# Kernel optimization log

Measured on AMD Instinct MI355X. Metric: run time of the kernel, lower is better.

Reference implementation:

```python
import jax, jax.numpy as jnp
import numpy as np

N = 50000   # n_nodes
E = 800000  # n_edges (avg degree 16)
D = 128     # d_model == hidden_dim
N_LAYERS = 3


def _xavier(key, fan_in, fan_out):
    limit = float(np.sqrt(6.0 / (fan_in + fan_out)))
    return jax.random.uniform(key, (fan_in, fan_out), jnp.float32, -limit, limit)


def setup_inputs() -> dict:
    key = jax.random.key(0)
    ks = jax.random.split(key, 2 + 2 * N_LAYERS)
    x = jax.random.normal(ks[0], (N, D), jnp.float32)
    edge_index = jax.random.randint(ks[1], (2, E), 0, N, jnp.int32)
    inp = {"x": x, "edge_index": edge_index}
    for i in range(N_LAYERS):
        inp[f"W{i}"] = _xavier(ks[2 + 2 * i], D, D)
        inp[f"b{i}"] = jax.random.uniform(ks[3 + 2 * i], (D,), jnp.float32, -0.1, 0.1)
    return inp


def _gcn_forward(x, src, dst, norm, Ws, bs):
    n = x.shape[0]
    h = x
    for i, (W, b) in enumerate(zip(Ws, bs)):
        m = (h @ W)[src] * norm[:, None]                       # [E+N, D] gather + scale
        h = jax.ops.segment_sum(m, dst, num_segments=n) + b    # scatter-add aggregate
        if i < len(Ws) - 1:
            h = jax.nn.relu(h)
    return h + x                                               # residual


def reference(x, edge_index, W0, b0, W1, b1, W2, b2):
    n = x.shape[0]
    loop = jnp.arange(n, dtype=edge_index.dtype)
    src = jnp.concatenate([edge_index[0], loop])  # add self-loops (GCNConv default)
    dst = jnp.concatenate([edge_index[1], loop])
    deg = jax.ops.segment_sum(jnp.ones_like(dst, x.dtype), dst, num_segments=n)
    dinv = jax.lax.rsqrt(deg)                     # deg >= 1 due to self-loops
    norm = dinv[src] * dinv[dst]                  # symmetric GCN normalization
    return _gcn_forward(x, src, dst, norm, (W0, W1, W2), (b0, b1, b2))
```

## Files before the change

kernel.cpp:

```cpp
#include <hip/hip_runtime.h>
#include <hip/hip_bf16.h>

#define D 128
#define BCAP 64


__device__ __forceinline__ unsigned short f2bf_rtne(float f) {
    unsigned int u = __float_as_uint(f);
    u += 0x7fffu + ((u >> 16) & 1u);
    return (unsigned short)(u >> 16);
}

__device__ __forceinline__ float bf_lo(unsigned int u) { return __uint_as_float(u << 16); }
__device__ __forceinline__ float bf_hi(unsigned int u) { return __uint_as_float(u & 0xffff0000u); }


__global__ void fill_bucket_kernel(const int* __restrict__ src, const int* __restrict__ dst,
                                   int* __restrict__ cnt, int* __restrict__ bucket, int E) {
    int e = blockIdx.x * blockDim.x + threadIdx.x;
    if (e >= E) return;
    int s = src[e];
    int d = dst[e];
    int pos = atomicAdd(&cnt[d], 1);
    if (pos < BCAP) bucket[((size_t)d << 6) + pos] = s;
}

__global__ void dinv_kernel(const int* __restrict__ cnt, float* __restrict__ dinv, int n) {
    int i = blockIdx.x * blockDim.x + threadIdx.x;
    if (i < n) dinv[i] = rsqrtf((float)cnt[i] + 1.0f);
}


#define TM 64

__global__ __launch_bounds__(256) void gemm128_kernel(const float* __restrict__ h,
                                                      const float* __restrict__ W,
                                                      unsigned short* __restrict__ out, int n) {
    __shared__ float sh[TM * D];
    const int tid = threadIdx.x;
    const int nbase = blockIdx.x * TM;

#pragma unroll
    for (int i = 0; i < 8; ++i) {
        int fi = tid + i * 256;
        int node = nbase + (fi >> 5);
        float4 v = make_float4(0.f, 0.f, 0.f, 0.f);
        if (node < n) v = *(const float4*)&h[(size_t)node * D + ((fi & 31) << 2)];
        *(float4*)&sh[fi << 2] = v;
    }
    __syncthreads();

    const int c4 = (tid & 31) << 2;
    const int ng = tid >> 5;
    const float* shb = &sh[(ng * 8) * D];

    float4 acc[8];
#pragma unroll
    for (int j = 0; j < 8; ++j) acc[j] = make_float4(0.f, 0.f, 0.f, 0.f);

    for (int k = 0; k < D; k += 4) {
        float4 w0 = *(const float4*)&W[(size_t)(k + 0) * D + c4];
        float4 w1 = *(const float4*)&W[(size_t)(k + 1) * D + c4];
        float4 w2 = *(const float4*)&W[(size_t)(k + 2) * D + c4];
        float4 w3 = *(const float4*)&W[(size_t)(k + 3) * D + c4];
#pragma unroll
        for (int j = 0; j < 8; ++j) {
            float4 hv = *(const float4*)&shb[j * D + k];
            acc[j].x = fmaf(hv.x, w0.x, acc[j].x); acc[j].y = fmaf(hv.x, w0.y, acc[j].y);
            acc[j].z = fmaf(hv.x, w0.z, acc[j].z); acc[j].w = fmaf(hv.x, w0.w, acc[j].w);
            acc[j].x = fmaf(hv.y, w1.x, acc[j].x); acc[j].y = fmaf(hv.y, w1.y, acc[j].y);
            acc[j].z = fmaf(hv.y, w1.z, acc[j].z); acc[j].w = fmaf(hv.y, w1.w, acc[j].w);
            acc[j].x = fmaf(hv.z, w2.x, acc[j].x); acc[j].y = fmaf(hv.z, w2.y, acc[j].y);
            acc[j].z = fmaf(hv.z, w2.z, acc[j].z); acc[j].w = fmaf(hv.z, w2.w, acc[j].w);
            acc[j].x = fmaf(hv.w, w3.x, acc[j].x); acc[j].y = fmaf(hv.w, w3.y, acc[j].y);
            acc[j].z = fmaf(hv.w, w3.z, acc[j].z); acc[j].w = fmaf(hv.w, w3.w, acc[j].w);
        }
    }

#pragma unroll
    for (int j = 0; j < 8; ++j) {
        int node = nbase + ng * 8 + j;
        if (node < n) {
            ushort4 p;
            p.x = f2bf_rtne(acc[j].x);
            p.y = f2bf_rtne(acc[j].y);
            p.z = f2bf_rtne(acc[j].z);
            p.w = f2bf_rtne(acc[j].w);
            *(ushort4*)&out[(size_t)node * D + c4] = p;
        }
    }
}


__global__ __launch_bounds__(256) void gather_kernel(const int* __restrict__ cnt,
                                                     const int* __restrict__ bucket,
                                                     const unsigned short* __restrict__ hW,
                                                     const float* __restrict__ dinv,
                                                     const float* __restrict__ b,
                                                     const float* __restrict__ x,
                                                     float* __restrict__ out,
                                                     int n, int final_layer) {
    int node = blockIdx.x * 8 + (threadIdx.x >> 5);
    if (node >= n) return;
    const int f = (threadIdx.x & 31) << 2;
    const int* row = bucket + ((size_t)node << 6);
    int len = cnt[node];
    if (len > BCAP) len = BCAP;
    const int len8 = len & ~7;

    float4 acc0 = make_float4(0.f, 0.f, 0.f, 0.f);
    float4 acc1 = make_float4(0.f, 0.f, 0.f, 0.f);
    int k = 0;
    for (; k < len8; k += 8) {
        int4 sa = *(const int4*)&row[k];
        int4 sb = *(const int4*)&row[k + 4];
        float n0 = dinv[sa.x], n1 = dinv[sa.y], n2 = dinv[sa.z], n3 = dinv[sa.w];
        float n4 = dinv[sb.x], n5 = dinv[sb.y], n6 = dinv[sb.z], n7 = dinv[sb.w];
        uint2 u0 = *(const uint2*)&hW[(size_t)sa.x * D + f];
        uint2 u1 = *(const uint2*)&hW[(size_t)sa.y * D + f];
        uint2 u2 = *(const uint2*)&hW[(size_t)sa.z * D + f];
        uint2 u3 = *(const uint2*)&hW[(size_t)sa.w * D + f];
        uint2 u4 = *(const uint2*)&hW[(size_t)sb.x * D + f];
        uint2 u5 = *(const uint2*)&hW[(size_t)sb.y * D + f];
        uint2 u6 = *(const uint2*)&hW[(size_t)sb.z * D + f];
        uint2 u7 = *(const uint2*)&hW[(size_t)sb.w * D + f];
        acc0.x = fmaf(bf_lo(u0.x), n0, acc0.x); acc0.y = fmaf(bf_hi(u0.x), n0, acc0.y);
        acc0.z = fmaf(bf_lo(u0.y), n0, acc0.z); acc0.w = fmaf(bf_hi(u0.y), n0, acc0.w);
        acc1.x = fmaf(bf_lo(u1.x), n1, acc1.x); acc1.y = fmaf(bf_hi(u1.x), n1, acc1.y);
        acc1.z = fmaf(bf_lo(u1.y), n1, acc1.z); acc1.w = fmaf(bf_hi(u1.y), n1, acc1.w);
        acc0.x = fmaf(bf_lo(u2.x), n2, acc0.x); acc0.y = fmaf(bf_hi(u2.x), n2, acc0.y);
        acc0.z = fmaf(bf_lo(u2.y), n2, acc0.z); acc0.w = fmaf(bf_hi(u2.y), n2, acc0.w);
        acc1.x = fmaf(bf_lo(u3.x), n3, acc1.x); acc1.y = fmaf(bf_hi(u3.x), n3, acc1.y);
        acc1.z = fmaf(bf_lo(u3.y), n3, acc1.z); acc1.w = fmaf(bf_hi(u3.y), n3, acc1.w);
        acc0.x = fmaf(bf_lo(u4.x), n4, acc0.x); acc0.y = fmaf(bf_hi(u4.x), n4, acc0.y);
        acc0.z = fmaf(bf_lo(u4.y), n4, acc0.z); acc0.w = fmaf(bf_hi(u4.y), n4, acc0.w);
        acc1.x = fmaf(bf_lo(u5.x), n5, acc1.x); acc1.y = fmaf(bf_hi(u5.x), n5, acc1.y);
        acc1.z = fmaf(bf_lo(u5.y), n5, acc1.z); acc1.w = fmaf(bf_hi(u5.y), n5, acc1.w);
        acc0.x = fmaf(bf_lo(u6.x), n6, acc0.x); acc0.y = fmaf(bf_hi(u6.x), n6, acc0.y);
        acc0.z = fmaf(bf_lo(u6.y), n6, acc0.z); acc0.w = fmaf(bf_hi(u6.y), n6, acc0.w);
        acc1.x = fmaf(bf_lo(u7.x), n7, acc1.x); acc1.y = fmaf(bf_hi(u7.x), n7, acc1.y);
        acc1.z = fmaf(bf_lo(u7.y), n7, acc1.z); acc1.w = fmaf(bf_hi(u7.y), n7, acc1.w);
    }
    for (; k < len; ++k) {
        int s = row[k];
        float ns = dinv[s];
        uint2 u = *(const uint2*)&hW[(size_t)s * D + f];
        acc0.x = fmaf(bf_lo(u.x), ns, acc0.x); acc0.y = fmaf(bf_hi(u.x), ns, acc0.y);
        acc0.z = fmaf(bf_lo(u.y), ns, acc0.z); acc0.w = fmaf(bf_hi(u.y), ns, acc0.w);
    }

    float di = dinv[node];
    uint2 uh = *(const uint2*)&hW[(size_t)node * D + f];
    float4 acc;
    acc.x = fmaf(bf_lo(uh.x), di, acc0.x + acc1.x);
    acc.y = fmaf(bf_hi(uh.x), di, acc0.y + acc1.y);
    acc.z = fmaf(bf_lo(uh.y), di, acc0.z + acc1.z);
    acc.w = fmaf(bf_hi(uh.y), di, acc0.w + acc1.w);

    float4 bv = *(const float4*)&b[f];
    float4 r;
    r.x = fmaf(acc.x, di, bv.x);
    r.y = fmaf(acc.y, di, bv.y);
    r.z = fmaf(acc.z, di, bv.z);
    r.w = fmaf(acc.w, di, bv.w);

    if (final_layer) {
        float4 xv = *(const float4*)&x[(size_t)node * D + f];
        r.x += xv.x; r.y += xv.y; r.z += xv.z; r.w += xv.w;
    } else {
        r.x = fmaxf(r.x, 0.f);
        r.y = fmaxf(r.y, 0.f);
        r.z = fmaxf(r.z, 0.f);
        r.w = fmaxf(r.w, 0.f);
    }
    *(float4*)&out[(size_t)node * D + f] = r;
}


extern "C" void kernel_launch(void* const* d_in, const int* in_sizes, int n_in,
                              void* d_out, int out_size, void* d_ws, size_t ws_size,
                              hipStream_t stream) {
    const float* x  = (const float*)d_in[0];
    const int*   ei = (const int*)d_in[1];
    const float* Ws[3] = {(const float*)d_in[2], (const float*)d_in[4], (const float*)d_in[6]};
    const float* bs[3] = {(const float*)d_in[3], (const float*)d_in[5], (const float*)d_in[7]};
    float* out = (float*)d_out;

    const int N = in_sizes[0] / D;
    const int E = in_sizes[1] / 2;
    const int* src = ei;
    const int* dst = ei + E;

    const size_t Na = ((size_t)N + 3) & ~(size_t)3;
    int*   cnt    = (int*)d_ws;
    int*   bucket = cnt + Na;
    float* dinv   = (float*)(bucket + (size_t)N * BCAP);
    unsigned short* A = (unsigned short*)(dinv + Na);
    float* B = (float*)(A + (((size_t)N * D + 7) & ~(size_t)7));

    hipMemsetAsync(cnt, 0, Na * sizeof(int), stream);
    fill_bucket_kernel<<<(E + 255) / 256, 256, 0, stream>>>(src, dst, cnt, bucket, E);
    dinv_kernel<<<(N + 255) / 256, 256, 0, stream>>>(cnt, dinv, N);

    const int gather_blocks = (N + 7) / 8;
    const float* h = x;
    for (int l = 0; l < 3; ++l) {
        gemm128_kernel<<<(N + TM - 1) / TM, 256, 0, stream>>>(h, Ws[l], A, N);
        float* dest = (l == 2) ? out : B;
        gather_kernel<<<gather_blocks, 256, 0, stream>>>(cnt, bucket, A, dinv,
                                                         bs[l], x, dest, N, l == 2);
        h = B;
    }
}
```

Before: 343.0 us.

## Fuse first GEMM with bucket fill, drop dinv kernel, store hidden as bf16

Interleaves first-layer GEMM tiles with edge-bucketing blocks in a single launch, so the independent preprocessing and layer-0 matmul share one grid. The separate dinv kernel and buffer are removed; the gather recomputes rsqrt from counts for each neighbor. Intermediate hidden activations are written in bf16 instead of fp32, which halves the write and GEMM-read traffic but adds an extra rounding step to the intermediates. The per-neighbor rsqrt adds some ALU work, and the gather reads cnt instead of dinv.

```diff
diff --git a/kernel.cpp b/kernel.cpp
--- a/kernel.cpp
+++ b/kernel.cpp
@@ -3,6 +3,7 @@
 
 #define D 128
 #define BCAP 64
+#define TM 64
 
 
 __device__ __forceinline__ unsigned short f2bf_rtne(float f) {
@@ -15,38 +16,38 @@
 __device__ __forceinline__ float bf_hi(unsigned int u) { return __uint_as_float(u & 0xffff0000u); }
 
 
-__global__ void fill_bucket_kernel(const int* __restrict__ src, const int* __restrict__ dst,
-                                   int* __restrict__ cnt, int* __restrict__ bucket, int E) {
-    int e = blockIdx.x * blockDim.x + threadIdx.x;
-    if (e >= E) return;
-    int s = src[e];
-    int d = dst[e];
-    int pos = atomicAdd(&cnt[d], 1);
-    if (pos < BCAP) bucket[((size_t)d << 6) + pos] = s;
-}
-
-__global__ void dinv_kernel(const int* __restrict__ cnt, float* __restrict__ dinv, int n) {
-    int i = blockIdx.x * blockDim.x + threadIdx.x;
-    if (i < n) dinv[i] = rsqrtf((float)cnt[i] + 1.0f);
-}
-
-
-#define TM 64
-
-__global__ __launch_bounds__(256) void gemm128_kernel(const float* __restrict__ h,
-                                                      const float* __restrict__ W,
-                                                      unsigned short* __restrict__ out, int n) {
-    __shared__ float sh[TM * D];
+__device__ __forceinline__ void gemm_tile(const float* __restrict__ h_f32,
+                                          const unsigned short* __restrict__ h_bf16,
+                                          const float* __restrict__ W,
+                                          unsigned short* __restrict__ out,
+                                          int n, int tile, float* sh) {
     const int tid = threadIdx.x;
-    const int nbase = blockIdx.x * TM;
-
-#pragma unroll
-    for (int i = 0; i < 8; ++i) {
-        int fi = tid + i * 256;
-        int node = nbase + (fi >> 5);
-        float4 v = make_float4(0.f, 0.f, 0.f, 0.f);
-        if (node < n) v = *(const float4*)&h[(size_t)node * D + ((fi & 31) << 2)];
-        *(float4*)&sh[fi << 2] = v;
+    const int nbase = tile * TM;
+
+    if (h_f32) {
+#pragma unroll
+        for (int i = 0; i < 8; ++i) {
+            int fi = tid + i * 256;
+            int node = nbase + (fi >> 5);
+            float4 v = make_float4(0.f, 0.f, 0.f, 0.f);
+            if (node < n) v = *(const float4*)&h_f32[(size_t)node * D + ((fi & 31) << 2)];
+            *(float4*)&sh[fi << 2] = v;
+        }
+    } else {
+#pragma unroll
+        for (int i = 0; i < 8; ++i) {
+            int fi = tid + i * 256;
+            int node = nbase + (fi >> 5);
+            float4 v = make_float4(0.f, 0.f, 0.f, 0.f);
+            if (node < n) {
+                ushort4 u = *(const ushort4*)&h_bf16[(size_t)node * D + ((fi & 31) << 2)];
+                v.x = __uint_as_float((unsigned)u.x << 16);
+                v.y = __uint_as_float((unsigned)u.y << 16);
+                v.z = __uint_as_float((unsigned)u.z << 16);
+                v.w = __uint_as_float((unsigned)u.w << 16);
+            }
+            *(float4*)&sh[fi << 2] = v;
+        }
     }
     __syncthreads();
 
@@ -92,19 +93,51 @@
 }
 
 
+__global__ __launch_bounds__(256) void fused_gemm0_fill_kernel(
+        const float* __restrict__ x, const float* __restrict__ W0,
+        unsigned short* __restrict__ A,
+        const int* __restrict__ src, const int* __restrict__ dst,
+        int* __restrict__ cnt, int* __restrict__ bucket,
+        int n, int E, int r, int gemmB, int fillB) {
+    __shared__ float sh[TM * D];
+    int b = blockIdx.x;
+    if (b % r == 0) {
+        int g = b / r;
+        if (g < gemmB) gemm_tile(x, nullptr, W0, A, n, g, sh);
+    } else {
+        int fid = b - b / r - 1;
+        if (fid >= fillB) return;
+        int e = fid * 256 + threadIdx.x;
+        if (e >= E) return;
+        int s = src[e];
+        int d = dst[e];
+        int pos = atomicAdd(&cnt[d], 1);
+        if (pos < BCAP) bucket[((size_t)d << 6) + pos] = s;
+    }
+}
+
+__global__ __launch_bounds__(256) void gemm128_kernel(const unsigned short* __restrict__ h,
+                                                      const float* __restrict__ W,
+                                                      unsigned short* __restrict__ out, int n) {
+    __shared__ float sh[TM * D];
+    gemm_tile(nullptr, h, W, out, n, blockIdx.x, sh);
+}
+
+
 __global__ __launch_bounds__(256) void gather_kernel(const int* __restrict__ cnt,
                                                      const int* __restrict__ bucket,
                                                      const unsigned short* __restrict__ hW,
-                                                     const float* __restrict__ dinv,
                                                      const float* __restrict__ b,
                                                      const float* __restrict__ x,
-                                                     float* __restrict__ out,
+                                                     float* __restrict__ out_f32,
+                                                     unsigned short* __restrict__ out_bf16,
                                                      int n, int final_layer) {
     int node = blockIdx.x * 8 + (threadIdx.x >> 5);
     if (node >= n) return;
     const int f = (threadIdx.x & 31) << 2;
     const int* row = bucket + ((size_t)node << 6);
     int len = cnt[node];
+    float di = rsqrtf((float)len + 1.0f);
     if (len > BCAP) len = BCAP;
     const int len8 = len & ~7;
 
@@ -114,8 +147,14 @@
     for (; k < len8; k += 8) {
         int4 sa = *(const int4*)&row[k];
         int4 sb = *(const int4*)&row[k + 4];
-        float n0 = dinv[sa.x], n1 = dinv[sa.y], n2 = dinv[sa.z], n3 = dinv[sa.w];
-        float n4 = dinv[sb.x], n5 = dinv[sb.y], n6 = dinv[sb.z], n7 = dinv[sb.w];
+        float n0 = rsqrtf((float)cnt[sa.x] + 1.0f);
+        float n1 = rsqrtf((float)cnt[sa.y] + 1.0f);
+        float n2 = rsqrtf((float)cnt[sa.z] + 1.0f);
+        float n3 = rsqrtf((float)cnt[sa.w] + 1.0f);
+        float n4 = rsqrtf((float)cnt[sb.x] + 1.0f);
+        float n5 = rsqrtf((float)cnt[sb.y] + 1.0f);
+        float n6 = rsqrtf((float)cnt[sb.z] + 1.0f);
+        float n7 = rsqrtf((float)cnt[sb.w] + 1.0f);
         uint2 u0 = *(const uint2*)&hW[(size_t)sa.x * D + f];
         uint2 u1 = *(const uint2*)&hW[(size_t)sa.y * D + f];
         uint2 u2 = *(const uint2*)&hW[(size_t)sa.z * D + f];
@@ -143,13 +182,12 @@
     }
     for (; k < len; ++k) {
         int s = row[k];
-        float ns = dinv[s];
+        float ns = rsqrtf((float)cnt[s] + 1.0f);
         uint2 u = *(const uint2*)&hW[(size_t)s * D + f];
         acc0.x = fmaf(bf_lo(u.x), ns, acc0.x); acc0.y = fmaf(bf_hi(u.x), ns, acc0.y);
         acc0.z = fmaf(bf_lo(u.y), ns, acc0.z); acc0.w = fmaf(bf_hi(u.y), ns, acc0.w);
     }
 
-    float di = dinv[node];
     uint2 uh = *(const uint2*)&hW[(size_t)node * D + f];
     float4 acc;
     acc.x = fmaf(bf_lo(uh.x), di, acc0.x + acc1.x);
@@ -167,13 +205,15 @@
     if (final_layer) {
         float4 xv = *(const float4*)&x[(size_t)node * D + f];
         r.x += xv.x; r.y += xv.y; r.z += xv.z; r.w += xv.w;
+        *(float4*)&out_f32[(size_t)node * D + f] = r;
     } else {
-        r.x = fmaxf(r.x, 0.f);
-        r.y = fmaxf(r.y, 0.f);
-        r.z = fmaxf(r.z, 0.f);
-        r.w = fmaxf(r.w, 0.f);
-    }
-    *(float4*)&out[(size_t)node * D + f] = r;
+        ushort4 p;
+        p.x = f2bf_rtne(fmaxf(r.x, 0.f));
+        p.y = f2bf_rtne(fmaxf(r.y, 0.f));
+        p.z = f2bf_rtne(fmaxf(r.z, 0.f));
+        p.w = f2bf_rtne(fmaxf(r.w, 0.f));
+        *(ushort4*)&out_bf16[(size_t)node * D + f] = p;
+    }
 }
 
 
@@ -192,23 +232,26 @@
     const int* dst = ei + E;
 
     const size_t Na = ((size_t)N + 3) & ~(size_t)3;
-    int*   cnt    = (int*)d_ws;
-    int*   bucket = cnt + Na;
-    float* dinv   = (float*)(bucket + (size_t)N * BCAP);
-    unsigned short* A = (unsigned short*)(dinv + Na);
-    float* B = (float*)(A + (((size_t)N * D + 7) & ~(size_t)7));
+    int* cnt    = (int*)d_ws;
+    int* bucket = cnt + Na;
+    unsigned short* A = (unsigned short*)(bucket + (size_t)N * BCAP);
+    unsigned short* B = A + (((size_t)N * D + 7) & ~(size_t)7);
+
+    const int gemmB = (N + TM - 1) / TM;
+    const int fillB = (E + 255) / 256;
+    const int r = 1 + (fillB + gemmB - 1) / gemmB;
+    const int fusedGrid = gemmB * r;
 
     hipMemsetAsync(cnt, 0, Na * sizeof(int), stream);
-    fill_bucket_kernel<<<(E + 255) / 256, 256, 0, stream>>>(src, dst, cnt, bucket, E);
-    dinv_kernel<<<(N + 255) / 256, 256, 0, stream>>>(cnt, dinv, N);
+    fused_gemm0_fill_kernel<<<fusedGrid, 256, 0, stream>>>(x, Ws[0], A, src, dst,
+                                                           cnt, bucket, N, E, r, gemmB, fillB);
 
     const int gather_blocks = (N + 7) / 8;
-    const float* h = x;
     for (int l = 0; l < 3; ++l) {
-        gemm128_kernel<<<(N + TM - 1) / TM, 256, 0, stream>>>(h, Ws[l], A, N);
-        float* dest = (l == 2) ? out : B;
-        gather_kernel<<<gather_blocks, 256, 0, stream>>>(cnt, bucket, A, dinv,
-                                                         bs[l], x, dest, N, l == 2);
-        h = B;
-    }
-}
+        if (l > 0) {
+            gemm128_kernel<<<gemmB, 256, 0, stream>>>(B, Ws[l], A, N);
+        }
+        gather_kernel<<<gather_blocks, 256, 0, stream>>>(cnt, bucket, A, bs[l], x,
+                                                         out, B, N, l == 2);
+    }
+}
```

New measurement: 333.4 us. 1.03x faster.
